# Performance work log

Hardware: AMD Instinct MI355X
Metric: run time of the kernel (lower is better)

Reference implementation:

```python
import jax, jax.numpy as jnp
import numpy as np

B, C, NX, NY = 8, 128, 256, 256
N = 32768

def setup_inputs() -> dict:
    key = jax.random.key(0)
    k1, k2 = jax.random.split(key)
    x = jax.random.normal(k1, (B, C, NX, NY), dtype=jnp.float32)
    coords = jax.random.uniform(k2, (B, N, 2), dtype=jnp.float32)
    return {"x": x, "coords": coords}

def reference(x, coords):
    b, c, nx, ny = x.shape
    # Match torch: scale by (dim-1), clamp to [0, dim], floor to int (nearest-lower gather).
    px = jnp.clip(coords[:, :, 1] * (nx - 1), 0, nx).astype(jnp.int32)  # (b, n)
    py = jnp.clip(coords[:, :, 0] * (ny - 1), 0, ny).astype(jnp.int32)  # (b, n)
    # Direct per-batch gather: out[b, c, n] = x[b, c, px[b,n], py[b,n]]
    flat_idx = px * ny + py                                             # (b, n)
    x_flat = x.reshape(b, c, nx * ny)                                   # (b, c, nx*ny)
    out = jnp.take_along_axis(x_flat, flat_idx[:, None, :], axis=2)     # (b, c, n)
    return out
```

## Files before the change

### kernel.cpp

```cpp
#include <hip/hip_runtime.h>

#define B_  8
#define C_  128
#define NX_ 256
#define NY_ 256
#define N_  32768
#define PLANE_ (NX_ * NY_)
#define XT_BYTES ((size_t)B_ * PLANE_ * C_ * 4)
#define BM_WORDS_PER_B (PLANE_ / 32)
#define BM_BYTES ((size_t)B_ * BM_WORDS_PER_B * 4)

typedef float f32x4 __attribute__((ext_vector_type(4)));
typedef float f32x2 __attribute__((ext_vector_type(2)));

__device__ __forceinline__ int sample_idx(const float* __restrict__ coords, int b, int n) {
    const float2 cc = *reinterpret_cast<const float2*>(coords + ((size_t)b * N_ + n) * 2);
    const int px = (int)fminf(fmaxf(cc.y * (float)(NX_ - 1), 0.0f), (float)NX_);
    const int py = (int)fminf(fmaxf(cc.x * (float)(NY_ - 1), 0.0f), (float)NY_);
    return min(px * NY_ + py, PLANE_ - 1);
}

__global__ __launch_bounds__(256) void mark_kernel(const float* __restrict__ coords,
                                                   unsigned* __restrict__ bm) {
    const int n = blockIdx.x * 256 + threadIdx.x;
    const int b = blockIdx.y;
    const int idx = sample_idx(coords, b, n);
    atomicOr(&bm[b * BM_WORDS_PER_B + (idx >> 5)], 1u << (idx & 31));
}

__global__ __launch_bounds__(256, 2) void transpose_kernel(const float* __restrict__ x,
                                                           const unsigned* __restrict__ bm,
                                                           float* __restrict__ xT) {
    __shared__ float tile[128][130];
    const int bid = blockIdx.x;
    const int b   = bid & 7;
    const int p0  = (bid >> 3) << 7;
    const int t   = threadIdx.x;
    const int w   = t >> 6, l = t & 63;
    const int q   = l & 31, h = l >> 5;

    const float* __restrict__ xb = x + (size_t)b * C_ * PLANE_ + p0;
    #pragma unroll
    for (int r = 0; r < 16; ++r) {
        const int c = r * 8 + w * 2 + h;
        const f32x4 v = __builtin_nontemporal_load(
            reinterpret_cast<const f32x4*>(xb + (size_t)c * PLANE_ + 4 * q));
        #pragma unroll
        for (int j = 0; j < 4; ++j) tile[4 * q + j][c] = v[j];
    }
    __syncthreads();

    float* __restrict__ xTb = xT + (size_t)b * PLANE_ * C_;
    const unsigned* __restrict__ bmb = bm + b * BM_WORDS_PER_B + (p0 >> 5);
    #pragma unroll
    for (int r = 0; r < 32; ++r) {
        const int p = r * 4 + w;
        if (bmb[p >> 5] & (1u << (p & 31))) {
            const f32x2 v2 = *reinterpret_cast<const f32x2*>(&tile[p][2 * l]);
            *reinterpret_cast<f32x2*>(&xTb[(size_t)(p0 + p) * C_ + 2 * l]) = v2;
        }
    }
}

__global__ __launch_bounds__(256, 2) void gather_kernel(const float* __restrict__ xT,
                                                        const float* __restrict__ coords,
                                                        float* __restrict__ out) {
    __shared__ float smp[C_][130];
    __shared__ int   sidx[128];
    const int bid = blockIdx.x;
    const int b   = bid & 7;
    const int n0  = (bid >> 3) << 7;
    const int t   = threadIdx.x;
    const int w   = t >> 6, l = t & 63;
    const int cq  = l & 31, sh = l >> 5;

    if (t < 128) sidx[t] = sample_idx(coords, b, n0 + t);
    __syncthreads();

    const float* __restrict__ xTb = xT + (size_t)b * PLANE_ * C_;
    #pragma unroll
    for (int r = 0; r < 16; ++r) {
        const int s = r * 8 + w * 2 + sh;
        const f32x4 v = *reinterpret_cast<const f32x4*>(xTb + (size_t)sidx[s] * C_ + 4 * cq);
        #pragma unroll
        for (int j = 0; j < 4; ++j) smp[4 * cq + j][s] = v[j];
    }
    __syncthreads();

    float* __restrict__ ob = out + (size_t)b * C_ * N_ + n0;
    #pragma unroll
    for (int r = 0; r < 32; ++r) {
        const int c = r * 4 + w;
        const f32x2 v2 = *reinterpret_cast<const f32x2*>(&smp[c][2 * l]);
        __builtin_nontemporal_store(v2, reinterpret_cast<f32x2*>(ob + (size_t)c * N_ + 2 * l));
    }
}

__global__ __launch_bounds__(256) void fallback_kernel(const float* __restrict__ x,
                                                       const float* __restrict__ coords,
                                                       float* __restrict__ out) {
    const int bid  = blockIdx.x;
    const int b    = bid & 7;
    const int rem  = bid >> 3;
    const int cg   = rem >> 7;
    const int nblk = rem & 127;
    const int n  = nblk * 256 + threadIdx.x;
    const int c0 = cg * 8;
    const int idx = sample_idx(coords, b, n);
    const float* __restrict__ xb = x + ((size_t)b * C_ + c0) * PLANE_ + idx;
    float* __restrict__ ob = out + ((size_t)b * C_ + c0) * N_ + n;
    #pragma unroll
    for (int i = 0; i < 8; ++i)
        __builtin_nontemporal_store(xb[(size_t)i * PLANE_], ob + (size_t)i * N_);
}

extern "C" void kernel_launch(void* const* d_in, const int* in_sizes, int n_in,
                              void* d_out, int out_size, void* d_ws, size_t ws_size,
                              hipStream_t stream) {
    const float* x      = (const float*)d_in[0];
    const float* coords = (const float*)d_in[1];
    float* out          = (float*)d_out;

    if (ws_size >= XT_BYTES + BM_BYTES) {
        float*    xT = (float*)d_ws;
        unsigned* bm = (unsigned*)((char*)d_ws + XT_BYTES);
        hipMemsetAsync(bm, 0, BM_BYTES, stream);
        mark_kernel<<<dim3(N_ / 256, B_), 256, 0, stream>>>(coords, bm);
        transpose_kernel<<<B_ * (PLANE_ / 128), 256, 0, stream>>>(x, bm, xT);
        gather_kernel<<<B_ * (N_ / 128), 256, 0, stream>>>(xT, coords, out);
    } else {
        fallback_kernel<<<B_ * 16 * 128, 256, 0, stream>>>(x, coords, out);
    }
}
```

Measured before the change: 441.9 us.

## Compact transposed samples via bitmap prefix-sum ranks instead of sparse plane layout

Adds a per-batch popcount prefix scan over the occupancy bitmap so that only sampled pixels are written densely (by rank) into the transposed buffer, and the gather looks up ranks instead of raw pixel indices. This packs the roughly 40% touched positions contiguously, which improves write and read locality and reduces the scattered cache/DRAM footprint. It adds a small serial scan kernel (8 blocks) and extra bitmap/base lookups in the transpose and gather kernels.

```diff
diff --git a/kernel.cpp b/kernel.cpp
--- a/kernel.cpp
+++ b/kernel.cpp
@@ -9,6 +9,7 @@
 #define XT_BYTES ((size_t)B_ * PLANE_ * C_ * 4)
 #define BM_WORDS_PER_B (PLANE_ / 32)
 #define BM_BYTES ((size_t)B_ * BM_WORDS_PER_B * 4)
+#define WS_NEED (XT_BYTES + 2 * BM_BYTES)
 
 typedef float f32x4 __attribute__((ext_vector_type(4)));
 typedef float f32x2 __attribute__((ext_vector_type(2)));
@@ -28,9 +29,33 @@
     atomicOr(&bm[b * BM_WORDS_PER_B + (idx >> 5)], 1u << (idx & 31));
 }
 
+__global__ __launch_bounds__(256) void scan_kernel(const unsigned* __restrict__ bm,
+                                                   unsigned* __restrict__ base) {
+    __shared__ unsigned ts[256];
+    const int b = blockIdx.x, t = threadIdx.x;
+    const unsigned* __restrict__ w = bm + b * BM_WORDS_PER_B + t * 8;
+    unsigned c[8], s = 0;
+    #pragma unroll
+    for (int j = 0; j < 8; ++j) { c[j] = s; s += __popc(w[j]); }
+    ts[t] = s;
+    __syncthreads();
+    #pragma unroll
+    for (int off = 1; off < 256; off <<= 1) {
+        const unsigned v = (t >= off) ? ts[t - off] : 0u;
+        __syncthreads();
+        ts[t] += v;
+        __syncthreads();
+    }
+    const unsigned pre = ts[t] - s;
+    unsigned* __restrict__ o = base + b * BM_WORDS_PER_B + t * 8;
+    #pragma unroll
+    for (int j = 0; j < 8; ++j) o[j] = pre + c[j];
+}
+
 __global__ __launch_bounds__(256, 2) void transpose_kernel(const float* __restrict__ x,
                                                            const unsigned* __restrict__ bm,
-                                                           float* __restrict__ xT) {
+                                                           const unsigned* __restrict__ base,
+                                                           float* __restrict__ xC) {
     __shared__ float tile[128][130];
     const int bid = blockIdx.x;
     const int b   = bid & 7;
@@ -50,19 +75,25 @@
     }
     __syncthreads();
 
-    float* __restrict__ xTb = xT + (size_t)b * PLANE_ * C_;
-    const unsigned* __restrict__ bmb = bm + b * BM_WORDS_PER_B + (p0 >> 5);
+    float* __restrict__ xCb = xC + (size_t)b * PLANE_ * C_;
+    const unsigned* __restrict__ bmb = bm + b * BM_WORDS_PER_B;
+    const unsigned* __restrict__ bsb = base + b * BM_WORDS_PER_B;
     #pragma unroll
     for (int r = 0; r < 32; ++r) {
-        const int p = r * 4 + w;
-        if (bmb[p >> 5] & (1u << (p & 31))) {
+        const int p  = r * 4 + w;
+        const int gp = p0 + p;
+        const unsigned bits = bmb[gp >> 5];
+        if (bits & (1u << (gp & 31))) {
+            const unsigned rank = bsb[gp >> 5] + __popc(bits & ((1u << (gp & 31)) - 1u));
             const f32x2 v2 = *reinterpret_cast<const f32x2*>(&tile[p][2 * l]);
-            *reinterpret_cast<f32x2*>(&xTb[(size_t)(p0 + p) * C_ + 2 * l]) = v2;
+            *reinterpret_cast<f32x2*>(&xCb[(size_t)rank * C_ + 2 * l]) = v2;
         }
     }
 }
 
-__global__ __launch_bounds__(256, 2) void gather_kernel(const float* __restrict__ xT,
+__global__ __launch_bounds__(256, 2) void gather_kernel(const float* __restrict__ xC,
+                                                        const unsigned* __restrict__ bm,
+                                                        const unsigned* __restrict__ base,
                                                         const float* __restrict__ coords,
                                                         float* __restrict__ out) {
     __shared__ float smp[C_][130];
@@ -74,14 +105,19 @@
     const int w   = t >> 6, l = t & 63;
     const int cq  = l & 31, sh = l >> 5;
 
-    if (t < 128) sidx[t] = sample_idx(coords, b, n0 + t);
+    if (t < 128) {
+        const int idx = sample_idx(coords, b, n0 + t);
+        const unsigned bits = bm[b * BM_WORDS_PER_B + (idx >> 5)];
+        sidx[t] = (int)(base[b * BM_WORDS_PER_B + (idx >> 5)] +
+                        __popc(bits & ((1u << (idx & 31)) - 1u)));
+    }
     __syncthreads();
 
-    const float* __restrict__ xTb = xT + (size_t)b * PLANE_ * C_;
+    const float* __restrict__ xCb = xC + (size_t)b * PLANE_ * C_;
     #pragma unroll
     for (int r = 0; r < 16; ++r) {
         const int s = r * 8 + w * 2 + sh;
-        const f32x4 v = *reinterpret_cast<const f32x4*>(xTb + (size_t)sidx[s] * C_ + 4 * cq);
+        const f32x4 v = *reinterpret_cast<const f32x4*>(xCb + (size_t)sidx[s] * C_ + 4 * cq);
         #pragma unroll
         for (int j = 0; j < 4; ++j) smp[4 * cq + j][s] = v[j];
     }
@@ -121,13 +157,15 @@
     const float* coords = (const float*)d_in[1];
     float* out          = (float*)d_out;
 
-    if (ws_size >= XT_BYTES + BM_BYTES) {
-        float*    xT = (float*)d_ws;
-        unsigned* bm = (unsigned*)((char*)d_ws + XT_BYTES);
+    if (ws_size >= WS_NEED) {
+        float*    xC   = (float*)d_ws;
+        unsigned* bm   = (unsigned*)((char*)d_ws + XT_BYTES);
+        unsigned* base = (unsigned*)((char*)d_ws + XT_BYTES + BM_BYTES);
         hipMemsetAsync(bm, 0, BM_BYTES, stream);
         mark_kernel<<<dim3(N_ / 256, B_), 256, 0, stream>>>(coords, bm);
-        transpose_kernel<<<B_ * (PLANE_ / 128), 256, 0, stream>>>(x, bm, xT);
-        gather_kernel<<<B_ * (N_ / 128), 256, 0, stream>>>(xT, coords, out);
+        scan_kernel<<<B_, 256, 0, stream>>>(bm, base);
+        transpose_kernel<<<B_ * (PLANE_ / 128), 256, 0, stream>>>(x, bm, base, xC);
+        gather_kernel<<<B_ * (N_ / 128), 256, 0, stream>>>(xC, bm, base, coords, out);
     } else {
         fallback_kernel<<<B_ * 16 * 128, 256, 0, stream>>>(x, coords, out);
     }
```

Measured after the change: 446.1 us. No clear change (+1.0%).
